# Optimization experiments

Hardware: AMD Instinct MI355X
Metric: run time of the kernel (lower is better)

## Reference

```python
import jax, jax.numpy as jnp
import numpy as np

N = 100000      # nodes
E = 3200000     # edges (avg degree 32)
F_IN = 128      # num_node_features
H = 16          # hidden dim (fixed in module)
C = 2           # num_classes


def setup_inputs() -> dict:
    key = jax.random.key(0)
    k0, k1, k2, k3 = jax.random.split(key, 4)
    x = jax.random.normal(k0, (N, F_IN), dtype=jnp.float32)
    edge_index = jax.random.randint(k1, (2, E), 0, N, dtype=jnp.int32)
    # GCNConv params: weight (in,out) + bias (out,) per layer (glorot-ish scale)
    W1 = jax.random.normal(k2, (F_IN, H), dtype=jnp.float32) * (1.0 / np.sqrt(F_IN))
    b1 = jnp.zeros((H,), jnp.float32)
    W2 = jax.random.normal(k3, (H, C), dtype=jnp.float32) * (1.0 / np.sqrt(H))
    b2 = jnp.zeros((C,), jnp.float32)
    return {"x": x, "edge_index": edge_index, "W1": W1, "b1": b1, "W2": W2, "b2": b2}


def _gcn_conv(x, W, b, src, dst, n):
    # GCNConv: h = D^{-1/2}(A+I)D^{-1/2} (x W) + b, with self-loops in src/dst
    h = x @ W                                   # [n, out]
    deg = jax.ops.segment_sum(jnp.ones_like(dst, dtype=h.dtype), dst, num_segments=n)
    dinv = jnp.where(deg > 0, jax.lax.rsqrt(deg), 0.0)
    norm = dinv[src] * dinv[dst]                # [E+n]
    msg = h[src] * norm[:, None]                # gather + scale
    out = jax.ops.segment_sum(msg, dst, num_segments=n)  # scatter-add
    return out + b


def reference(x, edge_index, W1, b1, W2, b2):
    loops = jnp.arange(N, dtype=edge_index.dtype)
    src = jnp.concatenate([edge_index[0], loops])
    dst = jnp.concatenate([edge_index[1], loops])
    h = jax.nn.relu(_gcn_conv(x, W1, b1, src, dst, N))
    # F.dropout(training=False) in eval mode is identity
    out = _gcn_conv(h, W2, b2, src, dst, N)
    return jax.nn.log_softmax(out, axis=1)
```

## Files before the change

kernel.cpp:

```cpp
#include <hip/hip_runtime.h>
#include <hip/hip_bf16.h>

#define NN 100000
#define NE 3200000
#define FIN 128
#define HD 16
#define CD 2

#define BSH 8
#define BSPAN 256
#define NBKT 391
#define CHUNK 8192
#define NPB ((NE + CHUNK - 1) / CHUNK)

__device__ __forceinline__ float bf2f(ushort u) {
    union { float f; unsigned int i; } v; v.i = ((unsigned int)u) << 16; return v.f;
}
__device__ __forceinline__ ushort f2b(float f) {
    union { float f; unsigned int u; } v; v.f = f;
    unsigned int r = (v.u + 0x7FFFu + ((v.u >> 16) & 1u)) >> 16;
    return (ushort)r;
}

__global__ __launch_bounds__(512) void k_cnt(const int* __restrict__ dst,
                                             int* __restrict__ cntmat) {
    __shared__ int h[NBKT];
    for (int i = threadIdx.x; i < NBKT; i += 512) h[i] = 0;
    __syncthreads();
    int cq = blockIdx.x * (CHUNK / 4);
    const int4* d4 = (const int4*)dst;
    #pragma unroll
    for (int j = 0; j < CHUNK / 2048; ++j) {
        int e4 = cq + j * 512 + threadIdx.x;
        if (e4 < NE / 4) {
            int4 d = d4[e4];
            atomicAdd(&h[d.x >> BSH], 1);
            atomicAdd(&h[d.y >> BSH], 1);
            atomicAdd(&h[d.z >> BSH], 1);
            atomicAdd(&h[d.w >> BSH], 1);
        }
    }
    __syncthreads();
    int* row = cntmat + (size_t)blockIdx.x * NBKT;
    for (int i = threadIdx.x; i < NBKT; i += 512) row[i] = h[i];
}

__global__ __launch_bounds__(256) void k_colscan(const int* __restrict__ cntmat,
                                                 int* __restrict__ relm,
                                                 int* __restrict__ btot) {
    __shared__ int sm[256];
    int j = blockIdx.x, t = threadIdx.x;
    int v[2];
    int b0 = t * 2;
    #pragma unroll
    for (int k = 0; k < 2; ++k) {
        int b = b0 + k;
        v[k] = (b < NPB) ? cntmat[(size_t)b * NBKT + j] : 0;
    }
    sm[t] = v[0] + v[1];
    __syncthreads();
    for (int off = 1; off < 256; off <<= 1) {
        int x = 0;
        if (t >= off) x = sm[t - off];
        __syncthreads();
        if (t >= off) sm[t] += x;
        __syncthreads();
    }
    int run = (t == 0) ? 0 : sm[t - 1];
    int* rrow = relm + (size_t)j * NPB;
    #pragma unroll
    for (int k = 0; k < 2; ++k) {
        int b = b0 + k;
        if (b < NPB) rrow[b] = run;
        run += v[k];
    }
    if (t == 255) btot[j] = sm[255];
}

__global__ __launch_bounds__(512) void k_scanb(const int* __restrict__ btot,
                                               int* __restrict__ boff) {
    __shared__ int sm[512];
    int t = threadIdx.x;
    sm[t] = (t < NBKT) ? btot[t] : 0;
    __syncthreads();
    for (int off = 1; off < 512; off <<= 1) {
        int v = 0;
        if (t >= off) v = sm[t - off];
        __syncthreads();
        if (t >= off) sm[t] += v;
        __syncthreads();
    }
    if (t < NBKT) boff[t] = t ? sm[t - 1] : 0;
    if (t == 511) boff[NBKT] = sm[511];
}

__global__ __launch_bounds__(512) void k_part(const int* __restrict__ src,
                                              const int* __restrict__ dst,
                                              const int* __restrict__ boff,
                                              const int* __restrict__ relm,
                                              unsigned int* __restrict__ csrb) {
    __shared__ int cur[NBKT];
    int b = blockIdx.x, t = threadIdx.x;
    for (int i = t; i < NBKT; i += 512)
        cur[i] = boff[i] + relm[(size_t)i * NPB + b];
    __syncthreads();
    int cq = b * (CHUNK / 4);
    const int4* s4 = (const int4*)src;
    const int4* d4 = (const int4*)dst;
    #pragma unroll
    for (int j = 0; j < CHUNK / 2048; ++j) {
        int e4 = cq + j * 512 + t;
        if (e4 < NE / 4) {
            int4 s = s4[e4];
            int4 d = d4[e4];
            int p;
            p = atomicAdd(&cur[d.x >> BSH], 1);
            csrb[p] = (unsigned)s.x | ((unsigned)(d.x & (BSPAN - 1)) << 17);
            p = atomicAdd(&cur[d.y >> BSH], 1);
            csrb[p] = (unsigned)s.y | ((unsigned)(d.y & (BSPAN - 1)) << 17);
            p = atomicAdd(&cur[d.z >> BSH], 1);
            csrb[p] = (unsigned)s.z | ((unsigned)(d.z & (BSPAN - 1)) << 17);
            p = atomicAdd(&cur[d.w >> BSH], 1);
            csrb[p] = (unsigned)s.w | ((unsigned)(d.w & (BSPAN - 1)) << 17);
        }
    }
}

__global__ __launch_bounds__(512) void k_sortb(const int* __restrict__ boff,
                                               const unsigned int* __restrict__ csrb,
                                               int* __restrict__ csr2,
                                               int* __restrict__ rowptr,
                                               float* __restrict__ dinv) {
    __shared__ int cnt[BSPAN];
    __shared__ int sc[BSPAN];
    __shared__ int cur[BSPAN];
    int b = blockIdx.x, t = threadIdx.x;
    if (t < BSPAN) cnt[t] = 0;
    __syncthreads();
    int e0 = boff[b], e1 = boff[b + 1];
    for (int e = e0 + t; e < e1; e += 512) atomicAdd(&cnt[csrb[e] >> 17], 1);
    __syncthreads();
    if (t < BSPAN) sc[t] = cnt[t];
    __syncthreads();
    for (int off = 1; off < BSPAN; off <<= 1) {
        int v = 0;
        if (t < BSPAN && t >= off) v = sc[t - off];
        __syncthreads();
        if (t < BSPAN && t >= off) sc[t] += v;
        __syncthreads();
    }
    if (t < BSPAN) {
        int ex = e0 + (t ? sc[t - 1] : 0);
        cur[t] = ex;
        int node = b * BSPAN + t;
        if (node < NN) {
            rowptr[node] = ex;
            dinv[node] = rsqrtf((float)cnt[t] + 1.0f);
        }
    }
    if (b == 0 && t == 0) rowptr[NN] = boff[NBKT];
    __syncthreads();
    for (int e = e0 + t; e < e1; e += 512) {
        unsigned p = csrb[e];
        int pos = atomicAdd(&cur[p >> 17], 1);
        csr2[pos] = (int)(p & 0x1FFFF);
    }
}

__global__ __launch_bounds__(256) void k_gemm1(const float* __restrict__ x,
                                               const float* __restrict__ W1,
                                               const float* __restrict__ dinv,
                                               ushort* __restrict__ h1b) {
    __shared__ float wsm[FIN][HD];
    for (int i = threadIdx.x; i < FIN * HD; i += 256) wsm[i >> 4][i & 15] = W1[i];
    __syncthreads();
    int t = blockIdx.x * 256 + threadIdx.x;
    int node = t >> 2;
    if (node >= NN) return;
    int g = (t & 3) * 4;
    const float4* xr = (const float4*)(x + (size_t)node * FIN);
    float a0 = 0.f, a1 = 0.f, a2 = 0.f, a3 = 0.f;
    #pragma unroll
    for (int k4 = 0; k4 < FIN / 4; ++k4) {
        float4 v = xr[k4];
        #pragma unroll
        for (int kk = 0; kk < 4; ++kk) {
            float vk = (kk == 0) ? v.x : (kk == 1) ? v.y : (kk == 2) ? v.z : v.w;
            float4 w = *(const float4*)&wsm[k4 * 4 + kk][g];
            a0 += vk * w.x;
            a1 += vk * w.y;
            a2 += vk * w.z;
            a3 += vk * w.w;
        }
    }
    float di = dinv[node];
    ushort4 r = {f2b(a0 * di), f2b(a1 * di), f2b(a2 * di), f2b(a3 * di)};
    *(ushort4*)(h1b + (size_t)node * HD + g) = r;
}

__global__ __launch_bounds__(256) void k_agg1(const int* __restrict__ rowptr,
                                              const int* __restrict__ csr2,
                                              const ushort* __restrict__ h1b,
                                              const float* __restrict__ dinv,
                                              const float* __restrict__ b1,
                                              const float* __restrict__ W2,
                                              float* __restrict__ g_s) {
    int wid = (blockIdx.x * 256 + threadIdx.x) >> 6;
    int lane = threadIdx.x & 63;
    int node = wid * 4 + (lane >> 4);
    if (node >= NN) return;
    int l16 = lane & 15;
    int slot = l16 >> 2;
    int fq = (lane & 3) * 4;
    int e0 = rowptr[node], e1 = rowptr[node + 1];
    float a0 = 0.f, a1 = 0.f, a2 = 0.f, a3 = 0.f;
    float c0 = 0.f, c1 = 0.f, c2 = 0.f, c3 = 0.f;
    int e = e0 + slot;
    for (; e + 4 < e1; e += 8) {
        int s0 = csr2[e];
        int s1 = csr2[e + 4];
        ushort4 u0 = *(const ushort4*)(h1b + (size_t)s0 * HD + fq);
        ushort4 u1 = *(const ushort4*)(h1b + (size_t)s1 * HD + fq);
        a0 += bf2f(u0.x); a1 += bf2f(u0.y); a2 += bf2f(u0.z); a3 += bf2f(u0.w);
        c0 += bf2f(u1.x); c1 += bf2f(u1.y); c2 += bf2f(u1.z); c3 += bf2f(u1.w);
    }
    if (e < e1) {
        ushort4 u = *(const ushort4*)(h1b + (size_t)csr2[e] * HD + fq);
        a0 += bf2f(u.x); a1 += bf2f(u.y); a2 += bf2f(u.z); a3 += bf2f(u.w);
    }
    a0 += c0; a1 += c1; a2 += c2; a3 += c3;
    #pragma unroll
    for (int m = 4; m <= 8; m <<= 1) {
        a0 += __shfl_xor(a0, m, 64);
        a1 += __shfl_xor(a1, m, 64);
        a2 += __shfl_xor(a2, m, 64);
        a3 += __shfl_xor(a3, m, 64);
    }
    if (slot == 0) {
        float di = dinv[node];
        ushort4 us = *(const ushort4*)(h1b + (size_t)node * HD + fq);
        float v0 = fmaxf(di * (a0 + bf2f(us.x)) + b1[fq],     0.f);
        float v1 = fmaxf(di * (a1 + bf2f(us.y)) + b1[fq + 1], 0.f);
        float v2 = fmaxf(di * (a2 + bf2f(us.z)) + b1[fq + 2], 0.f);
        float v3 = fmaxf(di * (a3 + bf2f(us.w)) + b1[fq + 3], 0.f);
        float p0 = v0 * W2[fq * 2]       + v1 * W2[(fq + 1) * 2]
                 + v2 * W2[(fq + 2) * 2] + v3 * W2[(fq + 3) * 2];
        float p1 = v0 * W2[fq * 2 + 1]       + v1 * W2[(fq + 1) * 2 + 1]
                 + v2 * W2[(fq + 2) * 2 + 1] + v3 * W2[(fq + 3) * 2 + 1];
        p0 += __shfl_xor(p0, 1, 64); p0 += __shfl_xor(p0, 2, 64);
        p1 += __shfl_xor(p1, 1, 64); p1 += __shfl_xor(p1, 2, 64);
        if (l16 == 0) {
            float2 r = {p0 * di, p1 * di};
            *(float2*)(g_s + (size_t)node * 2) = r;
        }
    }
}

__global__ __launch_bounds__(256) void k_agg2(const int* __restrict__ rowptr,
                                              const int* __restrict__ csr2,
                                              const float* __restrict__ g_s,
                                              const float* __restrict__ dinv,
                                              const float* __restrict__ b2,
                                              float* __restrict__ out) {
    int wid = (blockIdx.x * 256 + threadIdx.x) >> 6;
    int lane = threadIdx.x & 63;
    int node = wid * 4 + (lane >> 4);
    if (node >= NN) return;
    int l16 = lane & 15;
    int slot = l16 >> 1, f = lane & 1;
    int e0 = rowptr[node], e1 = rowptr[node + 1];
    float acc = 0.f;
    for (int e = e0 + slot; e < e1; e += 8)
        acc += g_s[(size_t)csr2[e] * 2 + f];
    #pragma unroll
    for (int m = 2; m <= 8; m <<= 1) acc += __shfl_xor(acc, m, 64);
    if (slot == 0) {
        float di = dinv[node];
        float o = di * (acc + g_s[(size_t)node * 2 + f]) + b2[f];
        float other = __shfl_xor(o, 1, 64);
        float mx = fmaxf(o, other);
        float l = mx + logf(__expf(o - mx) + __expf(other - mx));
        out[(size_t)node * 2 + f] = o - l;
    }
}

extern "C" void kernel_launch(void* const* d_in, const int* in_sizes, int n_in,
                              void* d_out, int out_size, void* d_ws, size_t ws_size,
                              hipStream_t stream) {
    const float* x   = (const float*)d_in[0];
    const int* ei    = (const int*)d_in[1];
    const int* src   = ei;
    const int* dst   = ei + NE;
    const float* W1  = (const float*)d_in[2];
    const float* b1  = (const float*)d_in[3];
    const float* W2  = (const float*)d_in[4];
    const float* b2  = (const float*)d_in[5];
    float* out = (float*)d_out;

    char* w = (char*)d_ws;
    float* dinv        = (float*)w;          w += NN * 4;
    int*   btot        = (int*)w;            w += NBKT * 4;
    int*   boff        = (int*)w;            w += (NBKT + 1) * 4;
    int*   rowptr      = (int*)w;            w += (NN + 1) * 4;
    int*   cntmat      = (int*)w;            w += (size_t)NPB * NBKT * 4;
    int*   relm        = (int*)w;            w += (size_t)NBKT * NPB * 4;
    unsigned int* csrb = (unsigned int*)w;   w += (size_t)NE * 4;
    int*   csr2        = (int*)w;            w += (size_t)NE * 4;
    ushort* h1b        = (ushort*)w;         w += (size_t)NN * HD * 2;
    float* g_s         = (float*)w;          w += NN * CD * 4;

    k_cnt    <<<NPB, 512, 0, stream>>>(dst, cntmat);
    k_colscan<<<NBKT, 256, 0, stream>>>(cntmat, relm, btot);
    k_scanb  <<<1, 512, 0, stream>>>(btot, boff);
    k_part   <<<NPB, 512, 0, stream>>>(src, dst, boff, relm, csrb);
    k_sortb  <<<NBKT, 512, 0, stream>>>(boff, csrb, csr2, rowptr, dinv);
    k_gemm1  <<<(NN * 4 + 255) / 256, 256, 0, stream>>>(x, W1, dinv, h1b);
    k_agg1   <<<(NN * 16 + 255) / 256, 256, 0, stream>>>(rowptr, csr2, h1b, dinv, b1, W2, g_s);
    k_agg2   <<<(NN * 16 + 255) / 256, 256, 0, stream>>>(rowptr, csr2, g_s, dinv, b2, out);
}
```

Measured before the change: 210.2 us.

## Replace per-node CSR sort with bucket-local shared-memory atomic aggregation

Drops the second counting sort that built a full CSR (rowptr/csr2) and instead aggregates each 256-node destination bucket directly from the bucketed edge list, using float atomics into a shared-memory accumulator. A lighter kernel now computes only the degrees. This removes one scatter pass over all edges and the writes and reads of csr2. In exchange, each block issues 16 LDS atomics per edge with possible contention on popular nodes. The grid also shrinks to 391 blocks, which may underuse the GPU, and the summation order becomes nondeterministic.

```diff
diff --git a/kernel.cpp b/kernel.cpp
--- a/kernel.cpp
+++ b/kernel.cpp
@@ -15,6 +15,12 @@
 
 __device__ __forceinline__ float bf2f(ushort u) {
     union { float f; unsigned int i; } v; v.i = ((unsigned int)u) << 16; return v.f;
+}
+__device__ __forceinline__ float lo2f(unsigned int u) {
+    union { float f; unsigned int i; } v; v.i = u << 16; return v.f;
+}
+__device__ __forceinline__ float hi2f(unsigned int u) {
+    union { float f; unsigned int i; } v; v.i = u & 0xFFFF0000u; return v.f;
 }
 __device__ __forceinline__ ushort f2b(float f) {
     union { float f; unsigned int u; } v; v.f = f;
@@ -126,44 +132,19 @@
     }
 }
 
-__global__ __launch_bounds__(512) void k_sortb(const int* __restrict__ boff,
-                                               const unsigned int* __restrict__ csrb,
-                                               int* __restrict__ csr2,
-                                               int* __restrict__ rowptr,
-                                               float* __restrict__ dinv) {
+__global__ __launch_bounds__(512) void k_deg(const int* __restrict__ boff,
+                                             const unsigned int* __restrict__ csrb,
+                                             float* __restrict__ dinv) {
     __shared__ int cnt[BSPAN];
-    __shared__ int sc[BSPAN];
-    __shared__ int cur[BSPAN];
     int b = blockIdx.x, t = threadIdx.x;
     if (t < BSPAN) cnt[t] = 0;
     __syncthreads();
     int e0 = boff[b], e1 = boff[b + 1];
     for (int e = e0 + t; e < e1; e += 512) atomicAdd(&cnt[csrb[e] >> 17], 1);
     __syncthreads();
-    if (t < BSPAN) sc[t] = cnt[t];
-    __syncthreads();
-    for (int off = 1; off < BSPAN; off <<= 1) {
-        int v = 0;
-        if (t < BSPAN && t >= off) v = sc[t - off];
-        __syncthreads();
-        if (t < BSPAN && t >= off) sc[t] += v;
-        __syncthreads();
-    }
     if (t < BSPAN) {
-        int ex = e0 + (t ? sc[t - 1] : 0);
-        cur[t] = ex;
         int node = b * BSPAN + t;
-        if (node < NN) {
-            rowptr[node] = ex;
-            dinv[node] = rsqrtf((float)cnt[t] + 1.0f);
-        }
-    }
-    if (b == 0 && t == 0) rowptr[NN] = boff[NBKT];
-    __syncthreads();
-    for (int e = e0 + t; e < e1; e += 512) {
-        unsigned p = csrb[e];
-        int pos = atomicAdd(&cur[p >> 17], 1);
-        csr2[pos] = (int)(p & 0x1FFFF);
+        if (node < NN) dinv[node] = rsqrtf((float)cnt[t] + 1.0f);
     }
 }
 
@@ -198,89 +179,98 @@
     *(ushort4*)(h1b + (size_t)node * HD + g) = r;
 }
 
-__global__ __launch_bounds__(256) void k_agg1(const int* __restrict__ rowptr,
-                                              const int* __restrict__ csr2,
-                                              const ushort* __restrict__ h1b,
-                                              const float* __restrict__ dinv,
-                                              const float* __restrict__ b1,
-                                              const float* __restrict__ W2,
-                                              float* __restrict__ g_s) {
-    int wid = (blockIdx.x * 256 + threadIdx.x) >> 6;
-    int lane = threadIdx.x & 63;
-    int node = wid * 4 + (lane >> 4);
-    if (node >= NN) return;
-    int l16 = lane & 15;
-    int slot = l16 >> 2;
-    int fq = (lane & 3) * 4;
-    int e0 = rowptr[node], e1 = rowptr[node + 1];
-    float a0 = 0.f, a1 = 0.f, a2 = 0.f, a3 = 0.f;
-    float c0 = 0.f, c1 = 0.f, c2 = 0.f, c3 = 0.f;
-    int e = e0 + slot;
-    for (; e + 4 < e1; e += 8) {
-        int s0 = csr2[e];
-        int s1 = csr2[e + 4];
-        ushort4 u0 = *(const ushort4*)(h1b + (size_t)s0 * HD + fq);
-        ushort4 u1 = *(const ushort4*)(h1b + (size_t)s1 * HD + fq);
-        a0 += bf2f(u0.x); a1 += bf2f(u0.y); a2 += bf2f(u0.z); a3 += bf2f(u0.w);
-        c0 += bf2f(u1.x); c1 += bf2f(u1.y); c2 += bf2f(u1.z); c3 += bf2f(u1.w);
-    }
-    if (e < e1) {
-        ushort4 u = *(const ushort4*)(h1b + (size_t)csr2[e] * HD + fq);
-        a0 += bf2f(u.x); a1 += bf2f(u.y); a2 += bf2f(u.z); a3 += bf2f(u.w);
-    }
-    a0 += c0; a1 += c1; a2 += c2; a3 += c3;
-    #pragma unroll
-    for (int m = 4; m <= 8; m <<= 1) {
-        a0 += __shfl_xor(a0, m, 64);
-        a1 += __shfl_xor(a1, m, 64);
-        a2 += __shfl_xor(a2, m, 64);
-        a3 += __shfl_xor(a3, m, 64);
-    }
-    if (slot == 0) {
+__global__ __launch_bounds__(512) void k_aggs1(const int* __restrict__ boff,
+                                               const unsigned int* __restrict__ csrb,
+                                               const ushort* __restrict__ h1b,
+                                               const float* __restrict__ dinv,
+                                               const float* __restrict__ b1,
+                                               const float* __restrict__ W2,
+                                               float* __restrict__ g_s) {
+    __shared__ float acc[BSPAN][HD + 1];
+    __shared__ float w2s[HD * 2];
+    __shared__ float b1s[HD];
+    int b = blockIdx.x, t = threadIdx.x;
+    for (int i = t; i < BSPAN * (HD + 1); i += 512) ((float*)acc)[i] = 0.f;
+    if (t < HD * 2) w2s[t] = W2[t];
+    else if (t < HD * 3) b1s[t - HD * 2] = b1[t - HD * 2];
+    __syncthreads();
+    int e0 = boff[b], e1 = boff[b + 1];
+    for (int e = e0 + t; e < e1; e += 512) {
+        unsigned p = csrb[e];
+        int s = p & 0x1FFFF;
+        float* a = acc[p >> 17];
+        const uint4* r = (const uint4*)(h1b + (size_t)s * HD);
+        uint4 u0 = r[0];
+        uint4 u1 = r[1];
+        atomicAdd(a + 0,  lo2f(u0.x)); atomicAdd(a + 1,  hi2f(u0.x));
+        atomicAdd(a + 2,  lo2f(u0.y)); atomicAdd(a + 3,  hi2f(u0.y));
+        atomicAdd(a + 4,  lo2f(u0.z)); atomicAdd(a + 5,  hi2f(u0.z));
+        atomicAdd(a + 6,  lo2f(u0.w)); atomicAdd(a + 7,  hi2f(u0.w));
+        atomicAdd(a + 8,  lo2f(u1.x)); atomicAdd(a + 9,  hi2f(u1.x));
+        atomicAdd(a + 10, lo2f(u1.y)); atomicAdd(a + 11, hi2f(u1.y));
+        atomicAdd(a + 12, lo2f(u1.z)); atomicAdd(a + 13, hi2f(u1.z));
+        atomicAdd(a + 14, lo2f(u1.w)); atomicAdd(a + 15, hi2f(u1.w));
+    }
+    __syncthreads();
+    int loc = t >> 1, half = t & 1;
+    int node = b * BSPAN + loc;
+    if (node < NN) {
         float di = dinv[node];
-        ushort4 us = *(const ushort4*)(h1b + (size_t)node * HD + fq);
-        float v0 = fmaxf(di * (a0 + bf2f(us.x)) + b1[fq],     0.f);
-        float v1 = fmaxf(di * (a1 + bf2f(us.y)) + b1[fq + 1], 0.f);
-        float v2 = fmaxf(di * (a2 + bf2f(us.z)) + b1[fq + 2], 0.f);
-        float v3 = fmaxf(di * (a3 + bf2f(us.w)) + b1[fq + 3], 0.f);
-        float p0 = v0 * W2[fq * 2]       + v1 * W2[(fq + 1) * 2]
-                 + v2 * W2[(fq + 2) * 2] + v3 * W2[(fq + 3) * 2];
-        float p1 = v0 * W2[fq * 2 + 1]       + v1 * W2[(fq + 1) * 2 + 1]
-                 + v2 * W2[(fq + 2) * 2 + 1] + v3 * W2[(fq + 3) * 2 + 1];
-        p0 += __shfl_xor(p0, 1, 64); p0 += __shfl_xor(p0, 2, 64);
-        p1 += __shfl_xor(p1, 1, 64); p1 += __shfl_xor(p1, 2, 64);
-        if (l16 == 0) {
+        const uint4 sv = *(const uint4*)(h1b + (size_t)node * HD + half * 8);
+        float s0 = lo2f(sv.x), s1 = hi2f(sv.x), s2 = lo2f(sv.y), s3 = hi2f(sv.y);
+        float s4 = lo2f(sv.z), s5 = hi2f(sv.z), s6 = lo2f(sv.w), s7 = hi2f(sv.w);
+        const float* a = acc[loc] + half * 8;
+        const float* bb = b1s + half * 8;
+        const float* ww = w2s + half * 16;
+        float sf[8] = {s0, s1, s2, s3, s4, s5, s6, s7};
+        float p0 = 0.f, p1 = 0.f;
+        #pragma unroll
+        for (int k = 0; k < 8; ++k) {
+            float v = fmaxf(di * (a[k] + sf[k]) + bb[k], 0.f);
+            p0 += v * ww[k * 2];
+            p1 += v * ww[k * 2 + 1];
+        }
+        p0 += __shfl_xor(p0, 1, 64);
+        p1 += __shfl_xor(p1, 1, 64);
+        if (half == 0) {
             float2 r = {p0 * di, p1 * di};
             *(float2*)(g_s + (size_t)node * 2) = r;
         }
     }
 }
 
-__global__ __launch_bounds__(256) void k_agg2(const int* __restrict__ rowptr,
-                                              const int* __restrict__ csr2,
-                                              const float* __restrict__ g_s,
-                                              const float* __restrict__ dinv,
-                                              const float* __restrict__ b2,
-                                              float* __restrict__ out) {
-    int wid = (blockIdx.x * 256 + threadIdx.x) >> 6;
-    int lane = threadIdx.x & 63;
-    int node = wid * 4 + (lane >> 4);
-    if (node >= NN) return;
-    int l16 = lane & 15;
-    int slot = l16 >> 1, f = lane & 1;
-    int e0 = rowptr[node], e1 = rowptr[node + 1];
-    float acc = 0.f;
-    for (int e = e0 + slot; e < e1; e += 8)
-        acc += g_s[(size_t)csr2[e] * 2 + f];
-    #pragma unroll
-    for (int m = 2; m <= 8; m <<= 1) acc += __shfl_xor(acc, m, 64);
-    if (slot == 0) {
-        float di = dinv[node];
-        float o = di * (acc + g_s[(size_t)node * 2 + f]) + b2[f];
-        float other = __shfl_xor(o, 1, 64);
-        float mx = fmaxf(o, other);
-        float l = mx + logf(__expf(o - mx) + __expf(other - mx));
-        out[(size_t)node * 2 + f] = o - l;
+__global__ __launch_bounds__(512) void k_aggs2(const int* __restrict__ boff,
+                                               const unsigned int* __restrict__ csrb,
+                                               const float* __restrict__ g_s,
+                                               const float* __restrict__ dinv,
+                                               const float* __restrict__ b2,
+                                               float* __restrict__ out) {
+    __shared__ float acc[BSPAN * 3];
+    int b = blockIdx.x, t = threadIdx.x;
+    for (int i = t; i < BSPAN * 3; i += 512) acc[i] = 0.f;
+    __syncthreads();
+    int e0 = boff[b], e1 = boff[b + 1];
+    for (int e = e0 + t; e < e1; e += 512) {
+        unsigned p = csrb[e];
+        int s = p & 0x1FFFF;
+        int loc = p >> 17;
+        float2 v = *(const float2*)(g_s + (size_t)s * 2);
+        atomicAdd(&acc[loc * 3], v.x);
+        atomicAdd(&acc[loc * 3 + 1], v.y);
+    }
+    __syncthreads();
+    if (t < BSPAN) {
+        int node = b * BSPAN + t;
+        if (node < NN) {
+            float di = dinv[node];
+            float2 sv = *(const float2*)(g_s + (size_t)node * 2);
+            float o0 = di * (acc[t * 3] + sv.x) + b2[0];
+            float o1 = di * (acc[t * 3 + 1] + sv.y) + b2[1];
+            float mx = fmaxf(o0, o1);
+            float l = mx + logf(__expf(o0 - mx) + __expf(o1 - mx));
+            float2 r = {o0 - l, o1 - l};
+            *(float2*)(out + (size_t)node * 2) = r;
+        }
     }
 }
 
@@ -301,11 +291,9 @@
     float* dinv        = (float*)w;          w += NN * 4;
     int*   btot        = (int*)w;            w += NBKT * 4;
     int*   boff        = (int*)w;            w += (NBKT + 1) * 4;
-    int*   rowptr      = (int*)w;            w += (NN + 1) * 4;
     int*   cntmat      = (int*)w;            w += (size_t)NPB * NBKT * 4;
     int*   relm        = (int*)w;            w += (size_t)NBKT * NPB * 4;
     unsigned int* csrb = (unsigned int*)w;   w += (size_t)NE * 4;
-    int*   csr2        = (int*)w;            w += (size_t)NE * 4;
     ushort* h1b        = (ushort*)w;         w += (size_t)NN * HD * 2;
     float* g_s         = (float*)w;          w += NN * CD * 4;
 
@@ -313,8 +301,8 @@
     k_colscan<<<NBKT, 256, 0, stream>>>(cntmat, relm, btot);
     k_scanb  <<<1, 512, 0, stream>>>(btot, boff);
     k_part   <<<NPB, 512, 0, stream>>>(src, dst, boff, relm, csrb);
-    k_sortb  <<<NBKT, 512, 0, stream>>>(boff, csrb, csr2, rowptr, dinv);
+    k_deg    <<<NBKT, 512, 0, stream>>>(boff, csrb, dinv);
     k_gemm1  <<<(NN * 4 + 255) / 256, 256, 0, stream>>>(x, W1, dinv, h1b);
-    k_agg1   <<<(NN * 16 + 255) / 256, 256, 0, stream>>>(rowptr, csr2, h1b, dinv, b1, W2, g_s);
-    k_agg2   <<<(NN * 16 + 255) / 256, 256, 0, stream>>>(rowptr, csr2, g_s, dinv, b2, out);
-}
+    k_aggs1  <<<NBKT, 512, 0, stream>>>(boff, csrb, h1b, dinv, b1, W2, g_s);
+    k_aggs2  <<<NBKT, 512, 0, stream>>>(boff, csrb, g_s, dinv, b2, out);
+}
```

New measurement: 533.0 us. 2.54x slower.
